# Performance work log

Measured on AMD Instinct MI355X. Metric: run time of the kernel, lower is better.

## Reference

```python
import jax, jax.numpy as jnp
import numpy as np

NUM_HEADS = 16
HEAD_DIM = 64  # embed_dim // num_heads
ROPE_BASE = 10000.0


def _apply_rope(x):
    # x: (B, H, S, D) -- standard rotate-half RoPE over the head dim
    B, H, S, D = x.shape
    inv_freq = 1.0 / (ROPE_BASE ** (jnp.arange(0, D, 2, dtype=jnp.float32) / D))  # (D/2,)
    ang = jnp.arange(S, dtype=jnp.float32)[:, None] * inv_freq[None, :]           # (S, D/2)
    emb = jnp.concatenate([ang, ang], axis=-1)                                     # (S, D)
    cos = jnp.cos(emb)[None, None].astype(x.dtype)
    sin = jnp.sin(emb)[None, None].astype(x.dtype)
    x1, x2 = x[..., : D // 2], x[..., D // 2 :]
    rot = jnp.concatenate([-x2, x1], axis=-1)
    return x * cos + rot * sin


def setup_inputs() -> dict:
    key = jax.random.key(0)
    ks = jax.random.split(key, 9)
    B, S, E, R = 2, 2048, 1024, 256
    s = 0.02
    return {
        "x": jax.random.normal(ks[0], (B, S, E), jnp.float32),
        "wq_down": jax.random.normal(ks[1], (R, E), jnp.float32) * s,
        "wk_rope": jax.random.normal(ks[2], (R, E), jnp.float32) * s,
        "wkv_down": jax.random.normal(ks[3], (R, E), jnp.float32) * s,
        "wq_rope": jax.random.normal(ks[4], (E, R), jnp.float32) * s,
        "wq_up": jax.random.normal(ks[5], (E, R), jnp.float32) * s,
        "wk_up": jax.random.normal(ks[6], (E, R), jnp.float32) * s,
        "wv_up": jax.random.normal(ks[7], (E, R), jnp.float32) * s,
        "wo": jax.random.normal(ks[8], (E, E), jnp.float32) * s,
    }


def _heads(t, B, S):
    # (B, S, E) -> (B, H, S, D)
    return t.reshape(B, S, NUM_HEADS, HEAD_DIM).transpose(0, 2, 1, 3)


def reference(x, wq_down, wk_rope, wkv_down, wq_rope, wq_up, wk_up, wv_up, wo):
    B, S, E = x.shape
    # low-rank query path
    q_lat = x @ wq_down.T                         # (B, S, R)
    q_r = _apply_rope(_heads(q_lat @ wq_rope.T, B, S))
    q_n = _heads(q_lat @ wq_up.T, B, S)
    q = jnp.concatenate([q_r, q_n], axis=-1)      # (B, H, S, 2D)
    # key rope path (separate latent)
    k_r = _apply_rope(_heads((x @ wk_rope.T) @ wk_up.T, B, S))
    # shared kv latent
    kv = x @ wkv_down.T                           # (B, S, R)
    k_n = _heads(kv @ wk_up.T, B, S)
    k = jnp.concatenate([k_r, k_n], axis=-1)      # (B, H, S, 2D)
    v = _heads(kv @ wv_up.T, B, S)                # (B, H, S, D)
    # causal SDPA, scale = 1/sqrt(q_dim) = 1/sqrt(2*HEAD_DIM)
    scale = 1.0 / jnp.sqrt(jnp.array(2 * HEAD_DIM, dtype=x.dtype))
    scores = jnp.einsum("bhqd,bhkd->bhqk", q, k) * scale
    mask = jnp.tril(jnp.ones((S, S), dtype=bool))
    scores = jnp.where(mask[None, None], scores, jnp.finfo(scores.dtype).min)
    attn = jax.nn.softmax(scores, axis=-1)
    y = jnp.einsum("bhqk,bhkd->bhqd", attn, v)    # (B, H, S, D)
    y = y.transpose(0, 2, 1, 3).reshape(B, S, E)
    return y @ wo.T
```

## Files before the change

### kernel.cpp

```cpp
#include <hip/hip_runtime.h>
#include <hip/hip_bf16.h>
#include <math.h>


typedef __attribute__((ext_vector_type(8))) short  short8;
typedef __attribute__((ext_vector_type(4))) float  floatx4;

static __device__ __forceinline__ unsigned short f2bf(float f) {
    __hip_bfloat16 h = __float2bfloat16(f);
    return *reinterpret_cast<unsigned short*>(&h);
}

#define GLL16(gp, lp) __builtin_amdgcn_global_load_lds( \
    (const __attribute__((address_space(1))) void*)(gp), \
    (__attribute__((address_space(3))) void*)(lp), 16, 0, 0)

struct CastDesc { const float* src; unsigned short* dst; int n4; };
struct CastArgs { CastDesc d[9]; };

__global__ __launch_bounds__(256) void cast_bf16_multi(CastArgs a)
{
    CastDesc dd = a.d[blockIdx.y];
    const int stride = gridDim.x * 256;
    for (int i = blockIdx.x * 256 + threadIdx.x; i < dd.n4; i += stride) {
        float4 v = ((const float4*)dd.src)[i];
        ushort4 o = make_ushort4(f2bf(v.x), f2bf(v.y), f2bf(v.z), f2bf(v.w));
        ((ushort4*)dd.dst)[i] = o;
    }
}

template<int MODE>
__global__ __launch_bounds__(256) void gemm_bf16(
    const unsigned short* __restrict__ A, int lda,
    const unsigned short* __restrict__ B0,
    const unsigned short* __restrict__ B1,
    const unsigned short* __restrict__ B2, int nspan, int ldb,
    void* __restrict__ Cout, int ldc, int K, float oscale)
{
    __shared__ __align__(16) unsigned short As[128 * 32];
    __shared__ __align__(16) unsigned short Bs[128 * 32];

    const int t    = threadIdx.x;
    const int w    = t >> 6;
    const int lane = t & 63;
    const int li   = lane & 15;
    const int quad = lane >> 4;
    const int wr   = w >> 1, wc = w & 1;
    const int m0   = blockIdx.y * 128;
    const int n0   = blockIdx.x * 128;

    const unsigned short* Bp = (n0 < nspan) ? B0 : ((n0 < 2 * nspan) ? B1 : B2);
    const int nb0 = n0 % nspan;

    const unsigned short* ga = A  + (size_t)(m0  + w * 32 + (lane >> 2)) * lda + (lane & 3) * 8;
    const unsigned short* gb = Bp + (size_t)(nb0 + w * 32 + (lane >> 2)) * ldb + (lane & 3) * 8;
    unsigned short* lA0 = &As[(w * 32) * 32];
    unsigned short* lA1 = &As[(w * 32 + 16) * 32];
    unsigned short* lB0 = &Bs[(w * 32) * 32];
    unsigned short* lB1 = &Bs[(w * 32 + 16) * 32];

    floatx4 acc[4][4];
    #pragma unroll
    for (int i = 0; i < 4; ++i)
        #pragma unroll
        for (int j = 0; j < 4; ++j)
            acc[i][j] = (floatx4){0.f, 0.f, 0.f, 0.f};

    for (int k0 = 0; k0 < K; k0 += 32) {
        __syncthreads();
        GLL16(ga + k0,            lA0);
        GLL16(ga + 16 * lda + k0, lA1);
        GLL16(gb + k0,            lB0);
        GLL16(gb + 16 * ldb + k0, lB1);
        __syncthreads();

        short8 af[4], bfr[4];
        #pragma unroll
        for (int mb = 0; mb < 4; ++mb)
            af[mb] = *(const short8*)&As[(wr * 64 + mb * 16 + li) * 32 + quad * 8];
        #pragma unroll
        for (int nb = 0; nb < 4; ++nb)
            bfr[nb] = *(const short8*)&Bs[(wc * 64 + nb * 16 + li) * 32 + quad * 8];
        #pragma unroll
        for (int mb = 0; mb < 4; ++mb)
            #pragma unroll
            for (int nb = 0; nb < 4; ++nb)
                acc[mb][nb] = __builtin_amdgcn_mfma_f32_16x16x32_bf16(
                    af[mb], bfr[nb], acc[mb][nb], 0, 0, 0);
    }

    if (MODE == 0) {
        float* C = (float*)Cout;
        #pragma unroll
        for (int mb = 0; mb < 4; ++mb)
            #pragma unroll
            for (int nb = 0; nb < 4; ++nb) {
                const int m = m0 + wr * 64 + mb * 16 + quad * 4;
                const int n = n0 + wc * 64 + nb * 16 + li;
                #pragma unroll
                for (int r = 0; r < 4; ++r)
                    C[(size_t)(m + r) * ldc + n] = acc[mb][nb][r] * oscale;
            }
    } else {
        unsigned short* C = (unsigned short*)Cout;
        #pragma unroll
        for (int mb = 0; mb < 4; ++mb)
            #pragma unroll
            for (int nb = 0; nb < 4; ++nb) {
                const int m = m0 + wr * 64 + mb * 16 + quad * 4;
                const int n = n0 + wc * 64 + nb * 16 + li;
                #pragma unroll
                for (int r = 0; r < 4; ++r)
                    C[(size_t)(m + r) * ldc + n] = f2bf(acc[mb][nb][r] * oscale);
            }
    }
}

__global__ __launch_bounds__(256) void gemm_qkv(
    const unsigned short* __restrict__ lat,
    const unsigned short* __restrict__ wqr, const unsigned short* __restrict__ wqu,
    const unsigned short* __restrict__ wku, const unsigned short* __restrict__ wvu,
    unsigned short* __restrict__ Qp, unsigned short* __restrict__ Kp,
    unsigned short* __restrict__ Vt, float qscale)
{
    __shared__ __align__(16) unsigned short As[128 * 32];
    __shared__ __align__(16) unsigned short Bs[128 * 32];

    const int t    = threadIdx.x;
    const int w    = t >> 6;
    const int lane = t & 63;
    const int li   = lane & 15;
    const int quad = lane >> 4;
    const int wr   = w >> 1, wc = w & 1;
    const int m0   = blockIdx.y * 128;
    const int n0   = blockIdx.x * 128;

    const unsigned short* Ap;
    const unsigned short* Bp;
    int nloc, seg;
    if (n0 < 1024)      { seg = 0; Ap = lat;       Bp = wqr; nloc = n0; }
    else if (n0 < 2048) { seg = 1; Ap = lat;       Bp = wqu; nloc = n0 - 1024; }
    else if (n0 < 3072) { seg = 2; Ap = lat + 256; Bp = wku; nloc = n0 - 2048; }
    else if (n0 < 4096) { seg = 3; Ap = lat + 512; Bp = wku; nloc = n0 - 3072; }
    else                { seg = 4; Ap = lat + 512; Bp = wvu; nloc = n0 - 4096; }
    const float oscale = (seg <= 1) ? qscale : 1.0f;

    const unsigned short* ga = Ap + (size_t)(m0   + w * 32 + (lane >> 2)) * 768 + (lane & 3) * 8;
    const unsigned short* gb = Bp + (size_t)(nloc + w * 32 + (lane >> 2)) * 256 + (lane & 3) * 8;
    unsigned short* lA0 = &As[(w * 32) * 32];
    unsigned short* lA1 = &As[(w * 32 + 16) * 32];
    unsigned short* lB0 = &Bs[(w * 32) * 32];
    unsigned short* lB1 = &Bs[(w * 32 + 16) * 32];

    floatx4 acc[4][4];
    #pragma unroll
    for (int i = 0; i < 4; ++i)
        #pragma unroll
        for (int j = 0; j < 4; ++j)
            acc[i][j] = (floatx4){0.f, 0.f, 0.f, 0.f};

    for (int k0 = 0; k0 < 256; k0 += 32) {
        __syncthreads();
        GLL16(ga + k0,           lA0);
        GLL16(ga + 16 * 768 + k0, lA1);
        GLL16(gb + k0,           lB0);
        GLL16(gb + 16 * 256 + k0, lB1);
        __syncthreads();

        short8 af[4], bfr[4];
        #pragma unroll
        for (int mb = 0; mb < 4; ++mb)
            af[mb] = *(const short8*)&As[(wr * 64 + mb * 16 + li) * 32 + quad * 8];
        #pragma unroll
        for (int nb = 0; nb < 4; ++nb)
            bfr[nb] = *(const short8*)&Bs[(wc * 64 + nb * 16 + li) * 32 + quad * 8];
        #pragma unroll
        for (int mb = 0; mb < 4; ++mb)
            #pragma unroll
            for (int nb = 0; nb < 4; ++nb)
                acc[mb][nb] = __builtin_amdgcn_mfma_f32_16x16x32_bf16(
                    af[mb], bfr[nb], acc[mb][nb], 0, 0, 0);
    }

    const int h = ((nloc + wc * 64) >> 6) & 15;

    if (seg == 0) {
        float invf[2];
        #pragma unroll
        for (int nb = 0; nb < 2; ++nb)
            invf[nb] = exp2f((float)(nb * 16 + li) * -0.4152410118609203f);
        #pragma unroll
        for (int mb = 0; mb < 4; ++mb) {
            const int m = m0 + wr * 64 + mb * 16 + quad * 4;
            const int b = m >> 11, s = m & 2047;
            #pragma unroll
            for (int nb = 0; nb < 2; ++nb) {
                const int dd = nb * 16 + li;
                size_t o = ((size_t)(b * 16 + h) * 2048 + s) * 128 + dd;
                #pragma unroll
                for (int r = 0; r < 4; ++r) {
                    float ang = (float)(s + r) * invf[nb];
                    float sn, cs;
                    sincosf(ang, &sn, &cs);
                    float x1 = acc[mb][nb][r], x2 = acc[mb][nb + 2][r];
                    Qp[o + (size_t)r * 128]      = f2bf((x1 * cs - x2 * sn) * oscale);
                    Qp[o + (size_t)r * 128 + 32] = f2bf((x2 * cs + x1 * sn) * oscale);
                }
            }
        }
    } else if (seg == 1) {
        #pragma unroll
        for (int mb = 0; mb < 4; ++mb)
            #pragma unroll
            for (int nb = 0; nb < 4; ++nb) {
                const int m = m0 + wr * 64 + mb * 16 + quad * 4;
                const int n = nloc + wc * 64 + nb * 16 + li;
                const int dn = n & 63;
                const int b = m >> 11, s = m & 2047;
                size_t o = ((size_t)(b * 16 + h) * 2048 + s) * 128 + 64 + dn;
                #pragma unroll
                for (int r = 0; r < 4; ++r)
                    Qp[o + (size_t)r * 128] = f2bf(acc[mb][nb][r] * oscale);
            }
    } else if (seg == 2) {
        float invf[2];
        #pragma unroll
        for (int nb = 0; nb < 2; ++nb)
            invf[nb] = exp2f((float)(nb * 16 + li) * -0.4152410118609203f);
        #pragma unroll
        for (int mb = 0; mb < 4; ++mb) {
            const int m = m0 + wr * 64 + mb * 16 + quad * 4;
            const int b = m >> 11, sba = m & 2047;
            #pragma unroll
            for (int nb = 0; nb < 2; ++nb) {
                const int dd = nb * 16 + li;
                const int d2 = dd + 32;
                #pragma unroll
                for (int r = 0; r < 4; ++r) {
                    const int s = sba + r;
                    float ang = (float)s * invf[nb];
                    float sn, cs;
                    sincosf(ang, &sn, &cs);
                    float x1 = acc[mb][nb][r], x2 = acc[mb][nb + 2][r];
                    size_t base = (size_t)(b * 16 + h) * 262144
                                + (size_t)(s >> 5) * 4096 + (size_t)(s & 31) * 8;
                    Kp[base + (dd >> 3) * 256 + (dd & 7)] = f2bf(x1 * cs - x2 * sn);
                    Kp[base + (d2 >> 3) * 256 + (d2 & 7)] = f2bf(x2 * cs + x1 * sn);
                }
            }
        }
    } else if (seg == 3) {
        #pragma unroll
        for (int mb = 0; mb < 4; ++mb)
            #pragma unroll
            for (int nb = 0; nb < 4; ++nb) {
                const int m = m0 + wr * 64 + mb * 16 + quad * 4;
                const int n = nloc + wc * 64 + nb * 16 + li;
                const int d = 64 + (n & 63);
                const int b = m >> 11, sba = m & 2047;
                #pragma unroll
                for (int r = 0; r < 4; ++r) {
                    const int s = sba + r;
                    size_t o = (size_t)(b * 16 + h) * 262144 + (size_t)(s >> 5) * 4096
                             + (size_t)(d >> 3) * 256 + (size_t)(s & 31) * 8 + (d & 7);
                    Kp[o] = f2bf(acc[mb][nb][r]);
                }
            }
    } else {
        #pragma unroll
        for (int mb = 0; mb < 4; ++mb)
            #pragma unroll
            for (int nb = 0; nb < 4; ++nb) {
                const int m = m0 + wr * 64 + mb * 16 + quad * 4;
                const int n = nloc + wc * 64 + nb * 16 + li;
                const int dn = n & 63;
                const int b = m >> 11, s = m & 2047;
                ushort4 st = make_ushort4(f2bf(acc[mb][nb][0]), f2bf(acc[mb][nb][1]),
                                          f2bf(acc[mb][nb][2]), f2bf(acc[mb][nb][3]));
                size_t o = (size_t)(b * 16 + h) * 131072 + (size_t)(s >> 5) * 2048
                         + (size_t)((s & 31) >> 3) * 512 + (size_t)dn * 8 + (s & 7);
                *(ushort4*)&Vt[o] = st;
            }
    }
}

__global__ __launch_bounds__(128, 8) void attn_mfma(
    const unsigned short* __restrict__ Qp, const unsigned short* __restrict__ Kp,
    const unsigned short* __restrict__ Vt, unsigned short* __restrict__ y)
{
    __shared__ __align__(16) unsigned short Ks[2][4096];
    __shared__ __align__(16) unsigned short PT[2][32][20];

    const int t    = threadIdx.x;
    const int w    = t >> 6;
    const int lane = t & 63;
    const int li   = lane & 15;
    const int quad = lane >> 4;

    const int blk = blockIdx.x;
    const int xcd = blk & 7;
    const int g   = blk >> 3;
    const int bh  = xcd + 8 * (g & 3);
    const int q32 = 63 - (g >> 2);
    const int b   = bh >> 4, h = bh & 15;

    const unsigned short* Kb = Kp + (size_t)bh * 262144;
    const unsigned short* Vb = Vt + (size_t)bh * 131072;
    const int qbase = q32 * 32 + w * 16;
    const int NKT   = q32 + 1;

    const unsigned short* Qb = Qp + ((size_t)bh * 2048 + qbase) * 128;
    short8 qf[4];
    #pragma unroll
    for (int kb = 0; kb < 4; ++kb)
        qf[kb] = *(const short8*)(Qb + (size_t)li * 128 + kb * 32 + quad * 8);

    short8 onesf;
    #pragma unroll
    for (int j = 0; j < 8; ++j) onesf[j] = (short)0x3F80;

    floatx4 o0 = {0.f,0.f,0.f,0.f}, o1 = {0.f,0.f,0.f,0.f};
    floatx4 o2 = {0.f,0.f,0.f,0.f}, o3 = {0.f,0.f,0.f,0.f};
    floatx4 ol = {0.f,0.f,0.f,0.f};

    auto stageK = [&](int kt, int buf) {
        const unsigned short* gkw = Kb + (size_t)kt * 4096 + w * 512 + (size_t)lane * 8;
        #pragma unroll
        for (int i = 0; i < 4; ++i)
            GLL16(gkw + i * 1024, &Ks[buf][w * 512 + i * 1024]);
    };
    auto loadV = [&](int kt, short8 vf[4]) {
        const unsigned short* gv = Vb + (size_t)kt * 2048 + quad * 512 + li * 8;
        #pragma unroll
        for (int nb = 0; nb < 4; ++nb)
            vf[nb] = *(const short8*)(gv + nb * 128);
    };
    auto compute = [&](int kt, int buf, short8 vf[4]) {
        const int kbase = kt * 32;
        floatx4 s0 = {0.f,0.f,0.f,0.f}, s1 = {0.f,0.f,0.f,0.f};
        #pragma unroll
        for (int kb = 0; kb < 4; ++kb) {
            short8 k0 = *(const short8*)&Ks[buf][(kb * 4 + quad) * 256 + li * 8];
            short8 k1 = *(const short8*)&Ks[buf][(kb * 4 + quad) * 256 + (16 + li) * 8];
            s0 = __builtin_amdgcn_mfma_f32_16x16x32_bf16(qf[kb], k0, s0, 0, 0, 0);
            s1 = __builtin_amdgcn_mfma_f32_16x16x32_bf16(qf[kb], k1, s1, 0, 0, 0);
        }
        unsigned short pe0[4], pe1[4];
        #pragma unroll
        for (int r = 0; r < 4; ++r) {
            const int qrow = qbase + quad * 4 + r;
            pe0[r] = (kbase + li      <= qrow) ? f2bf(__expf(s0[r])) : (unsigned short)0;
            pe1[r] = (kbase + 16 + li <= qrow) ? f2bf(__expf(s1[r])) : (unsigned short)0;
        }
        *(ushort4*)&PT[w][li][quad * 4]      = make_ushort4(pe0[0], pe0[1], pe0[2], pe0[3]);
        *(ushort4*)&PT[w][16 + li][quad * 4] = make_ushort4(pe1[0], pe1[1], pe1[2], pe1[3]);

        short8 pf;
        const unsigned short* pb = &PT[w][quad * 8][li];
        #pragma unroll
        for (int jj = 0; jj < 8; ++jj)
            pf[jj] = (short)pb[jj * 20];

        ol = __builtin_amdgcn_mfma_f32_16x16x32_bf16(pf, onesf, ol, 0, 0, 0);
        o0 = __builtin_amdgcn_mfma_f32_16x16x32_bf16(pf, vf[0], o0, 0, 0, 0);
        o1 = __builtin_amdgcn_mfma_f32_16x16x32_bf16(pf, vf[1], o1, 0, 0, 0);
        o2 = __builtin_amdgcn_mfma_f32_16x16x32_bf16(pf, vf[2], o2, 0, 0, 0);
        o3 = __builtin_amdgcn_mfma_f32_16x16x32_bf16(pf, vf[3], o3, 0, 0, 0);
    };

    short8 vfa[4], vfb[4];
    stageK(0, 0);
    loadV(0, vfa);

    int kt = 0;
    while (true) {
        __syncthreads();
        if (kt + 1 < NKT) { stageK(kt + 1, 1); loadV(kt + 1, vfb); }
        compute(kt, 0, vfa);
        ++kt; if (kt == NKT) break;
        __syncthreads();
        if (kt + 1 < NKT) { stageK(kt + 1, 0); loadV(kt + 1, vfa); }
        compute(kt, 1, vfb);
        ++kt; if (kt == NKT) break;
    }

    unsigned short* yb2 = y + ((size_t)b * 2048 + qbase + quad * 4) * 1024 + h * 64 + li;
    #pragma unroll
    for (int r = 0; r < 4; ++r) {
        const float linv = 1.0f / ol[r];
        yb2[(size_t)r * 1024 + 0]  = f2bf(o0[r] * linv);
        yb2[(size_t)r * 1024 + 16] = f2bf(o1[r] * linv);
        yb2[(size_t)r * 1024 + 32] = f2bf(o2[r] * linv);
        yb2[(size_t)r * 1024 + 48] = f2bf(o3[r] * linv);
    }
}

extern "C" void kernel_launch(void* const* d_in, const int* in_sizes, int n_in,
                              void* d_out, int out_size, void* d_ws, size_t ws_size,
                              hipStream_t stream)
{
    const float* x        = (const float*)d_in[0];
    const float* wq_down  = (const float*)d_in[1];
    const float* wk_rope  = (const float*)d_in[2];
    const float* wkv_down = (const float*)d_in[3];
    const float* wq_rope  = (const float*)d_in[4];
    const float* wq_up    = (const float*)d_in[5];
    const float* wk_up    = (const float*)d_in[6];
    const float* wv_up    = (const float*)d_in[7];
    const float* wo       = (const float*)d_in[8];
    float* out = (float*)d_out;

    char* wsb = (char*)d_ws;
    const size_t MB = 1u << 20;
    unsigned short* xb   = (unsigned short*)(wsb + 0 * MB);
    unsigned short* lat  = (unsigned short*)(wsb + 8 * MB);
    unsigned short* Qp   = (unsigned short*)(wsb + 14 * MB);
    unsigned short* Kp   = (unsigned short*)(wsb + 30 * MB);
    unsigned short* Vt   = (unsigned short*)(wsb + 46 * MB);
    unsigned short* yb   = (unsigned short*)(wsb + 54 * MB);
    unsigned short* wqd_b = (unsigned short*)(wsb + 62 * MB);
    unsigned short* wkr_b = (unsigned short*)(wsb + 63 * MB);
    unsigned short* wkd_b = (unsigned short*)(wsb + 64 * MB);
    unsigned short* wqr_b = (unsigned short*)(wsb + 65 * MB);
    unsigned short* wqu_b = (unsigned short*)(wsb + 66 * MB);
    unsigned short* wku_b = (unsigned short*)(wsb + 67 * MB);
    unsigned short* wvu_b = (unsigned short*)(wsb + 68 * MB);
    unsigned short* wo_b  = (unsigned short*)(wsb + 69 * MB);

    const float scale = 0.08838834764831845f;
    dim3 blk(256);

    CastArgs ca;
    ca.d[0] = { x,        xb,    4194304 / 4 };
    ca.d[1] = { wq_down,  wqd_b,  262144 / 4 };
    ca.d[2] = { wk_rope,  wkr_b,  262144 / 4 };
    ca.d[3] = { wkv_down, wkd_b,  262144 / 4 };
    ca.d[4] = { wq_rope,  wqr_b,  262144 / 4 };
    ca.d[5] = { wq_up,    wqu_b,  262144 / 4 };
    ca.d[6] = { wk_up,    wku_b,  262144 / 4 };
    ca.d[7] = { wv_up,    wvu_b,  262144 / 4 };
    ca.d[8] = { wo,       wo_b,  1048576 / 4 };
    cast_bf16_multi<<<dim3(128, 9), blk, 0, stream>>>(ca);

    gemm_bf16<3><<<dim3(6, 32), blk, 0, stream>>>(
        xb, 1024, wqd_b, wkr_b, wkd_b, 256, 1024, lat, 768, 1024, 1.f);

    gemm_qkv<<<dim3(40, 32), blk, 0, stream>>>(
        lat, wqr_b, wqu_b, wku_b, wvu_b, Qp, Kp, Vt, scale);

    attn_mfma<<<dim3(2048), dim3(128), 0, stream>>>(Qp, Kp, Vt, yb);

    gemm_bf16<0><<<dim3(8, 32), blk, 0, stream>>>(
        yb, 1024, wo_b, wo_b, wo_b, 1024, 1024, out, 1024, 1024, 1.f);
}
```

Measured before the change: 228.0 us.

## Shrink GEMM tiles to 64x64, widen attention blocks to 64 queries, skip masked tiles

```diff
diff --git a/kernel.cpp b/kernel.cpp
--- a/kernel.cpp
+++ b/kernel.cpp
@@ -30,24 +30,23 @@
 }
 
 template<int MODE>
-__global__ __launch_bounds__(256) void gemm_bf16(
+__global__ __launch_bounds__(128) void gemm64(
     const unsigned short* __restrict__ A, int lda,
     const unsigned short* __restrict__ B0,
     const unsigned short* __restrict__ B1,
     const unsigned short* __restrict__ B2, int nspan, int ldb,
     void* __restrict__ Cout, int ldc, int K, float oscale)
 {
-    __shared__ __align__(16) unsigned short As[128 * 32];
-    __shared__ __align__(16) unsigned short Bs[128 * 32];
+    __shared__ __align__(16) unsigned short As[64 * 32];
+    __shared__ __align__(16) unsigned short Bs[64 * 32];
 
     const int t    = threadIdx.x;
     const int w    = t >> 6;
     const int lane = t & 63;
     const int li   = lane & 15;
     const int quad = lane >> 4;
-    const int wr   = w >> 1, wc = w & 1;
-    const int m0   = blockIdx.y * 128;
-    const int n0   = blockIdx.x * 128;
+    const int m0   = blockIdx.y * 64;
+    const int n0   = blockIdx.x * 64;
 
     const unsigned short* Bp = (n0 < nspan) ? B0 : ((n0 < 2 * nspan) ? B1 : B2);
     const int nb0 = n0 % nspan;
@@ -59,9 +58,9 @@
     unsigned short* lB0 = &Bs[(w * 32) * 32];
     unsigned short* lB1 = &Bs[(w * 32 + 16) * 32];
 
-    floatx4 acc[4][4];
+    floatx4 acc[2][4];
     #pragma unroll
-    for (int i = 0; i < 4; ++i)
+    for (int i = 0; i < 2; ++i)
         #pragma unroll
         for (int j = 0; j < 4; ++j)
             acc[i][j] = (floatx4){0.f, 0.f, 0.f, 0.f};
@@ -74,15 +73,15 @@
         GLL16(gb + 16 * ldb + k0, lB1);
         __syncthreads();
 
-        short8 af[4], bfr[4];
-        #pragma unroll
-        for (int mb = 0; mb < 4; ++mb)
-            af[mb] = *(const short8*)&As[(wr * 64 + mb * 16 + li) * 32 + quad * 8];
+        short8 af[2], bfr[4];
+        #pragma unroll
+        for (int mb = 0; mb < 2; ++mb)
+            af[mb] = *(const short8*)&As[(w * 32 + mb * 16 + li) * 32 + quad * 8];
         #pragma unroll
         for (int nb = 0; nb < 4; ++nb)
-            bfr[nb] = *(const short8*)&Bs[(wc * 64 + nb * 16 + li) * 32 + quad * 8];
-        #pragma unroll
-        for (int mb = 0; mb < 4; ++mb)
+            bfr[nb] = *(const short8*)&Bs[(nb * 16 + li) * 32 + quad * 8];
+        #pragma unroll
+        for (int mb = 0; mb < 2; ++mb)
             #pragma unroll
             for (int nb = 0; nb < 4; ++nb)
                 acc[mb][nb] = __builtin_amdgcn_mfma_f32_16x16x32_bf16(
@@ -92,11 +91,11 @@
     if (MODE == 0) {
         float* C = (float*)Cout;
         #pragma unroll
-        for (int mb = 0; mb < 4; ++mb)
+        for (int mb = 0; mb < 2; ++mb)
             #pragma unroll
             for (int nb = 0; nb < 4; ++nb) {
-                const int m = m0 + wr * 64 + mb * 16 + quad * 4;
-                const int n = n0 + wc * 64 + nb * 16 + li;
+                const int m = m0 + w * 32 + mb * 16 + quad * 4;
+                const int n = n0 + nb * 16 + li;
                 #pragma unroll
                 for (int r = 0; r < 4; ++r)
                     C[(size_t)(m + r) * ldc + n] = acc[mb][nb][r] * oscale;
@@ -104,11 +103,11 @@
     } else {
         unsigned short* C = (unsigned short*)Cout;
         #pragma unroll
-        for (int mb = 0; mb < 4; ++mb)
+        for (int mb = 0; mb < 2; ++mb)
             #pragma unroll
             for (int nb = 0; nb < 4; ++nb) {
-                const int m = m0 + wr * 64 + mb * 16 + quad * 4;
-                const int n = n0 + wc * 64 + nb * 16 + li;
+                const int m = m0 + w * 32 + mb * 16 + quad * 4;
+                const int n = n0 + nb * 16 + li;
                 #pragma unroll
                 for (int r = 0; r < 4; ++r)
                     C[(size_t)(m + r) * ldc + n] = f2bf(acc[mb][nb][r] * oscale);
@@ -161,9 +160,9 @@
 
     for (int k0 = 0; k0 < 256; k0 += 32) {
         __syncthreads();
-        GLL16(ga + k0,           lA0);
+        GLL16(ga + k0,            lA0);
         GLL16(ga + 16 * 768 + k0, lA1);
-        GLL16(gb + k0,           lB0);
+        GLL16(gb + k0,            lB0);
         GLL16(gb + 16 * 256 + k0, lB1);
         __syncthreads();
 
@@ -284,12 +283,12 @@
     }
 }
 
-__global__ __launch_bounds__(128, 8) void attn_mfma(
+__global__ __launch_bounds__(256, 4) void attn_mfma(
     const unsigned short* __restrict__ Qp, const unsigned short* __restrict__ Kp,
     const unsigned short* __restrict__ Vt, unsigned short* __restrict__ y)
 {
     __shared__ __align__(16) unsigned short Ks[2][4096];
-    __shared__ __align__(16) unsigned short PT[2][32][20];
+    __shared__ __align__(16) unsigned short PT[4][640];
 
     const int t    = threadIdx.x;
     const int w    = t >> 6;
@@ -301,13 +300,14 @@
     const int xcd = blk & 7;
     const int g   = blk >> 3;
     const int bh  = xcd + 8 * (g & 3);
-    const int q32 = 63 - (g >> 2);
+    const int qt  = 31 - (g >> 2);
     const int b   = bh >> 4, h = bh & 15;
 
     const unsigned short* Kb = Kp + (size_t)bh * 262144;
     const unsigned short* Vb = Vt + (size_t)bh * 131072;
-    const int qbase = q32 * 32 + w * 16;
-    const int NKT   = q32 + 1;
+    const int qbase  = qt * 64 + w * 16;
+    const int NKT    = 2 * qt + 2;
+    const int lastkt = (qbase + 15) >> 5;
 
     const unsigned short* Qb = Qp + ((size_t)bh * 2048 + qbase) * 128;
     short8 qf[4];
@@ -323,11 +323,12 @@
     floatx4 o2 = {0.f,0.f,0.f,0.f}, o3 = {0.f,0.f,0.f,0.f};
     floatx4 ol = {0.f,0.f,0.f,0.f};
 
+    unsigned short* Pw = &PT[w][0];
+
     auto stageK = [&](int kt, int buf) {
-        const unsigned short* gkw = Kb + (size_t)kt * 4096 + w * 512 + (size_t)lane * 8;
-        #pragma unroll
-        for (int i = 0; i < 4; ++i)
-            GLL16(gkw + i * 1024, &Ks[buf][w * 512 + i * 1024]);
+        const unsigned short* gk = Kb + (size_t)kt * 4096 + w * 1024 + (size_t)lane * 8;
+        GLL16(gk,       &Ks[buf][w * 1024]);
+        GLL16(gk + 512, &Ks[buf][w * 1024 + 512]);
     };
     auto loadV = [&](int kt, short8 vf[4]) {
         const unsigned short* gv = Vb + (size_t)kt * 2048 + quad * 512 + li * 8;
@@ -335,7 +336,7 @@
         for (int nb = 0; nb < 4; ++nb)
             vf[nb] = *(const short8*)(gv + nb * 128);
     };
-    auto compute = [&](int kt, int buf, short8 vf[4]) {
+    auto compute = [&](int kt, int buf, short8 vf[4], bool maskTile) {
         const int kbase = kt * 32;
         floatx4 s0 = {0.f,0.f,0.f,0.f}, s1 = {0.f,0.f,0.f,0.f};
         #pragma unroll
@@ -345,21 +346,20 @@
             s0 = __builtin_amdgcn_mfma_f32_16x16x32_bf16(qf[kb], k0, s0, 0, 0, 0);
             s1 = __builtin_amdgcn_mfma_f32_16x16x32_bf16(qf[kb], k1, s1, 0, 0, 0);
         }
-        unsigned short pe0[4], pe1[4];
         #pragma unroll
         for (int r = 0; r < 4; ++r) {
-            const int qrow = qbase + quad * 4 + r;
-            pe0[r] = (kbase + li      <= qrow) ? f2bf(__expf(s0[r])) : (unsigned short)0;
-            pe1[r] = (kbase + 16 + li <= qrow) ? f2bf(__expf(s1[r])) : (unsigned short)0;
-        }
-        *(ushort4*)&PT[w][li][quad * 4]      = make_ushort4(pe0[0], pe0[1], pe0[2], pe0[3]);
-        *(ushort4*)&PT[w][16 + li][quad * 4] = make_ushort4(pe1[0], pe1[1], pe1[2], pe1[3]);
-
-        short8 pf;
-        const unsigned short* pb = &PT[w][quad * 8][li];
-        #pragma unroll
-        for (int jj = 0; jj < 8; ++jj)
-            pf[jj] = (short)pb[jj * 20];
+            const int i = quad * 4 + r;
+            unsigned int u0 = __float_as_uint(__expf(s0[r])) >> 16;
+            unsigned int u1 = __float_as_uint(__expf(s1[r])) >> 16;
+            if (maskTile) {
+                const int qrow = qbase + i;
+                u0 = (kbase + li      <= qrow) ? u0 : 0u;
+                u1 = (kbase + 16 + li <= qrow) ? u1 : 0u;
+            }
+            Pw[i * 40 + li]      = (unsigned short)u0;
+            Pw[i * 40 + 16 + li] = (unsigned short)u1;
+        }
+        short8 pf = *(const short8*)&Pw[li * 40 + quad * 8];
 
         ol = __builtin_amdgcn_mfma_f32_16x16x32_bf16(pf, onesf, ol, 0, 0, 0);
         o0 = __builtin_amdgcn_mfma_f32_16x16x32_bf16(pf, vf[0], o0, 0, 0, 0);
@@ -375,12 +375,18 @@
     int kt = 0;
     while (true) {
         __syncthreads();
-        if (kt + 1 < NKT) { stageK(kt + 1, 1); loadV(kt + 1, vfb); }
-        compute(kt, 0, vfa);
+        if (kt + 1 < NKT) {
+            stageK(kt + 1, 1);
+            if (kt + 1 <= lastkt) loadV(kt + 1, vfb);
+        }
+        if (kt <= lastkt) compute(kt, 0, vfa, kt == lastkt);
         ++kt; if (kt == NKT) break;
         __syncthreads();
-        if (kt + 1 < NKT) { stageK(kt + 1, 0); loadV(kt + 1, vfa); }
-        compute(kt, 1, vfb);
+        if (kt + 1 < NKT) {
+            stageK(kt + 1, 0);
+            if (kt + 1 <= lastkt) loadV(kt + 1, vfa);
+        }
+        if (kt <= lastkt) compute(kt, 1, vfb, kt == lastkt);
         ++kt; if (kt == NKT) break;
     }
 
@@ -428,6 +434,7 @@
     unsigned short* wo_b  = (unsigned short*)(wsb + 69 * MB);
 
     const float scale = 0.08838834764831845f;
+    const int BIG = 1 << 30;
     dim3 blk(256);
 
     CastArgs ca;
@@ -442,14 +449,14 @@
     ca.d[8] = { wo,       wo_b,  1048576 / 4 };
     cast_bf16_multi<<<dim3(128, 9), blk, 0, stream>>>(ca);
 
-    gemm_bf16<3><<<dim3(6, 32), blk, 0, stream>>>(
+    gemm64<3><<<dim3(12, 64), dim3(128), 0, stream>>>(
         xb, 1024, wqd_b, wkr_b, wkd_b, 256, 1024, lat, 768, 1024, 1.f);
 
     gemm_qkv<<<dim3(40, 32), blk, 0, stream>>>(
         lat, wqr_b, wqu_b, wku_b, wvu_b, Qp, Kp, Vt, scale);
 
-    attn_mfma<<<dim3(2048), dim3(128), 0, stream>>>(Qp, Kp, Vt, yb);
-
-    gemm_bf16<0><<<dim3(8, 32), blk, 0, stream>>>(
-        yb, 1024, wo_b, wo_b, wo_b, 1024, 1024, out, 1024, 1024, 1.f);
-}
+    attn_mfma<<<dim3(1024), blk, 0, stream>>>(Qp, Kp, Vt, yb);
+
+    gemm64<0><<<dim3(16, 64), dim3(128), 0, stream>>>(
+        yb, 1024, wo_b, wo_b, wo_b, BIG, 1024, out, 1024, 1024, 1.f);
+}
```

New measurement: 210.6 us. -7.6%, faster.
